# Performance work log

Measured on AMD Instinct MI355X. Metric: run time of the kernel, lower is better.

The kernel has to match this reference:

```python
import jax, jax.numpy as jnp
import numpy as np
from functools import partial

TAU = 2.0          # LIFNode default tau
V_TH = 1.0         # default v_threshold
ALPHA = 2.0        # SoftSign surrogate default alpha (unused in fwd; heaviside forward)

T, B, F = 256, 64, 1024


@jax.custom_vjp
def soft_sign_spike(x):
    # forward: heaviside; backward: SoftSign surrogate gradient
    return (x >= 0).astype(x.dtype)

def _sss_fwd(x):
    return (x >= 0).astype(x.dtype), x

def _sss_bwd(x, g):
    grad = g * (ALPHA / 2.0) / jnp.square(1.0 + jnp.abs(ALPHA * x))
    return (grad,)

soft_sign_spike.defvjp(_sss_fwd, _sss_bwd)


def setup_inputs() -> dict:
    key = jax.random.key(0)
    k1, k2 = jax.random.split(key)
    # binary input spikes, as an SNN would receive
    input_spikes = (jax.random.uniform(k1, (T, B, F)) < 0.5).astype(jnp.float32)
    # torch.nn.Linear weight [out_features, in_features], Kaiming-uniform-ish init
    bound = 1.0 / np.sqrt(F)
    W = jax.random.uniform(k2, (F, F), minval=-bound, maxval=bound, dtype=jnp.float32)
    return {"input_spikes": input_spikes, "W": W}


def reference(input_spikes, W):
    # batch the per-timestep Linear into one GEMM: y = x @ W.T
    cur = jnp.einsum("tbf,gf->tbg", input_spikes, W)  # [T, B, F]

    def step(v, x):
        # decay_input=True, v_reset=0: v = v + (x - v) / tau
        v = v + (x - v) / TAU
        s = soft_sign_spike(v - V_TH)
        # hard reset to v_reset=0 (detach_reset=False)
        v = (1.0 - s) * v
        return v, s

    v0 = jnp.zeros(cur.shape[1:], dtype=cur.dtype)
    _, out = jax.lax.scan(step, v0, cur)
    return out  # [T, B, F] output spikes
```

## Files before the change

kernel.cpp:

```cpp
#include <hip/hip_runtime.h>
#include <stdint.h>


#define T_STEPS 256
#define M_DIM 16384
#define N_DIM 1024
#define K_DIM 1024
#define PLANE 65536

typedef int v4i  __attribute__((ext_vector_type(4)));
typedef int v16i __attribute__((ext_vector_type(16)));
typedef unsigned int u32;
typedef unsigned long long u64;

#define AB_BYTES   (M_DIM * K_DIM)
#define AB_LIMB    AB_BYTES
#define WS_AB      (AB_BYTES + 4 * (1 << 20))
#define MT_BITS    (M_DIM * 128)
#define WS_MT      (MT_BITS + 4 * (1 << 20))

__device__ __forceinline__ void gload_lds16(const void* g, void* l) {
    __builtin_amdgcn_global_load_lds(
        (const __attribute__((address_space(1))) u32*)g,
        (__attribute__((address_space(3))) u32*)l, 16, 0, 0);
}

__global__ __launch_bounds__(256) void prep_bytes_f(const float* __restrict__ X,
                                                    uint4* __restrict__ af) {
    const int gid  = blockIdx.x * 256 + threadIdx.x;
    const int lane = gid & 63;
    const int fs   = gid >> 6;
    const int m    = (fs >> 5) * 32 + (lane & 31);
    const int k    = (fs & 31) * 32 + (lane >> 5) * 16;
    const float4* src = reinterpret_cast<const float4*>(X + (size_t)m * K_DIM + k);
    uint4 r;
    u32* pr = &r.x;
    #pragma unroll
    for (int q = 0; q < 4; ++q) {
        const float4 f = src[q];
        pr[q] = (f.x != 0.f ? 1u : 0u) | (f.y != 0.f ? 0x100u : 0u) |
                (f.z != 0.f ? 0x10000u : 0u) | (f.w != 0.f ? 0x1000000u : 0u);
    }
    af[gid] = r;
}

__global__ __launch_bounds__(256) void prep_limbs_f(const float* __restrict__ W,
                                                    char* __restrict__ bf) {
    const int gid  = blockIdx.x * 256 + threadIdx.x;
    const int lane = gid & 63;
    const int fs   = gid >> 6;
    const int n    = (fs >> 5) * 32 + (lane & 31);
    const int k    = (fs & 31) * 32 + (lane >> 5) * 16;
    const float* src = W + (size_t)n * K_DIM + k;
    u32 w0[4] = {}, w1[4] = {}, w2[4] = {}, w3[4] = {};
    #pragma unroll
    for (int e = 0; e < 16; ++e) {
        const double d = (double)src[e] * 34359738368.0;
        long long kq = llrint(d);
        const int8_t l0 = (int8_t)kq; kq = (kq - l0) >> 8;
        const int8_t l1 = (int8_t)kq; kq = (kq - l1) >> 8;
        const int8_t l2 = (int8_t)kq; kq = (kq - l2) >> 8;
        const int8_t l3 = (int8_t)kq;
        const int sh = (e & 3) * 8, wd = e >> 2;
        w0[wd] |= ((u32)(uint8_t)l0) << sh;
        w1[wd] |= ((u32)(uint8_t)l1) << sh;
        w2[wd] |= ((u32)(uint8_t)l2) << sh;
        w3[wd] |= ((u32)(uint8_t)l3) << sh;
    }
    char* base = bf + (size_t)fs * 4096 + lane * 16;
    *(uint4*)(base)        = make_uint4(w0[0], w0[1], w0[2], w0[3]);
    *(uint4*)(base + 1024) = make_uint4(w1[0], w1[1], w1[2], w1[3]);
    *(uint4*)(base + 2048) = make_uint4(w2[0], w2[1], w2[2], w2[3]);
    *(uint4*)(base + 3072) = make_uint4(w3[0], w3[1], w3[2], w3[3]);
}

__global__ __launch_bounds__(512, 4) void gemm_i8_w8(
    const char* __restrict__ af, const char* __restrict__ bf,
    float* __restrict__ out) {
    __shared__ __align__(16) char lds[2][16384];

    const int tid  = threadIdx.x;
    const int lane = tid & 63;
    const int w    = tid >> 6;
    const int l31  = lane & 31;
    const int lh   = lane >> 5;

    const int L   = blockIdx.x;
    const int xcd = L & 7;
    const int j   = L >> 3;
    const int bm  = xcd * 8 + (j & 7);
    const int bn  = j >> 3;

    v16i acc[4] = {};

    const char* gB = bf + (size_t)bn * 131072 + (size_t)(2 * w) * 1024 + lane * 16;

    const char* gA = af + (size_t)(bm * 8 + w) * 32768 + lane * 16;

    gload_lds16(gB,        (char*)lds[0] + (2 * w) * 1024 + lane * 16);
    gload_lds16(gB + 1024, (char*)lds[0] + (2 * w) * 1024 + 1024 + lane * 16);
    v4i aw = *(const v4i*)(gA);
    v4i an;
    __syncthreads();

    for (int c = 0; c < 8; ++c) {
        const char* rb = lds[c & 1];
        char* wb = (char*)lds[(c & 1) ^ 1];
        if (c < 7) {
            gload_lds16(gB + (size_t)(c + 1) * 16384,
                        wb + (2 * w) * 1024 + lane * 16);
            gload_lds16(gB + (size_t)(c + 1) * 16384 + 1024,
                        wb + (2 * w) * 1024 + 1024 + lane * 16);
        }
        #pragma unroll
        for (int ks = 0; ks < 4; ++ks) {
            const int kg = c * 4 + ks;
            if (kg + 1 < 32) an = *(const v4i*)(gA + (kg + 1) * 1024);
            #pragma unroll
            for (int lb = 0; lb < 4; ++lb) {
                const v4i b = *(const v4i*)(rb + (ks * 4 + lb) * 1024 + lane * 16);
                acc[lb] = __builtin_amdgcn_mfma_i32_32x32x32_i8(aw, b, acc[lb], 0, 0, 0);
            }
            aw = an;
        }
        __syncthreads();
    }

    const int n = bn * 32 + l31;
    #pragma unroll
    for (int r = 0; r < 16; ++r) {
        const double s = (double)acc[0][r] + 256.0 * (double)acc[1][r] +
                         65536.0 * (double)acc[2][r] +
                         16777216.0 * (double)acc[3][r];
        const float cur = (float)(s * 2.9103830456733704e-11);
        const int row = (r & 3) + 8 * (r >> 2) + 4 * lh;
        const int m = (bm * 8 + w) * 32 + row;
        out[(size_t)m * N_DIM + n] = cur;
    }
}

__device__ __forceinline__ v4i expand16(u32 sb) {
    v4i r;
    #pragma unroll
    for (int q = 0; q < 4; ++q) {
        const u32 x = (sb >> (4 * q)) & 0xFu;
        r[q] = (int)((x * 0x00204081u) & 0x01010101u);
    }
    return r;
}

__global__ __launch_bounds__(256) void prep_bits(const float* __restrict__ X,
                                                 u64* __restrict__ bits) {
    const int gid = blockIdx.x * 256 + threadIdx.x;
    const float x = X[gid];
    const u64 m = __ballot(x != 0.0f);
    if ((threadIdx.x & 63) == 0) bits[gid >> 6] = m;
}

__global__ __launch_bounds__(256) void prep_limbs(const float* __restrict__ W,
                                                  char* __restrict__ limbs) {
    const int gid = blockIdx.x * 256 + threadIdx.x;
    const double d = (double)W[gid] * 34359738368.0;
    long long k = llrint(d);
    const int8_t l0 = (int8_t)k; k = (k - l0) >> 8;
    const int8_t l1 = (int8_t)k; k = (k - l1) >> 8;
    const int8_t l2 = (int8_t)k; k = (k - l2) >> 8;
    const int8_t l3 = (int8_t)k;
    limbs[gid]                 = (char)l0;
    limbs[gid + (1 << 20)]     = (char)l1;
    limbs[gid + 2 * (1 << 20)] = (char)l2;
    limbs[gid + 3 * (1 << 20)] = (char)l3;
}

__global__ __launch_bounds__(256, 2) void gemm_i8_reg2(
    const u64* __restrict__ bits, const char* __restrict__ limbs,
    float* __restrict__ out) {
    __shared__ __align__(16) char lds[2][32768];
    const int tid  = threadIdx.x;
    const int lane = tid & 63;
    const int w    = tid >> 6;
    const int l31  = lane & 31;
    const int lh   = lane >> 5;
    const int bn   = blockIdx.x;
    const int bm   = blockIdx.y;
    v16i acc[2][4] = {};
    const char* gB[8];
    #pragma unroll
    for (int j = 0; j < 8; ++j) {
        const int id = w * 8 + j;
        const int lb = id & 3, ks32 = id >> 2;
        gB[j] = limbs + (size_t)lb * (1 << 20) +
                (size_t)(bn * 32 + l31) * 1024 + (size_t)(ks32 * 32 + lh * 16);
    }
    const int ldsbase = w * 8192 + lane * 16;
    const u64* aRow0 = bits + (size_t)(bm * 256 + w * 64 + l31) * 16;
    const u64* aRow1 = aRow0 + 32 * 16;
    u64 aw0[4], aw1[4], an0[4], an1[4];
    #pragma unroll
    for (int j = 0; j < 8; ++j) gload_lds16(gB[j], lds[0] + ldsbase + j * 1024);
    #pragma unroll
    for (int q = 0; q < 4; ++q) { aw0[q] = aRow0[q]; aw1[q] = aRow1[q]; }
    __syncthreads();
    char* rb = lds[0];
    char* wb = lds[1];
    for (int c = 0; c < 4; ++c) {
        if (c < 3) {
            #pragma unroll
            for (int j = 0; j < 8; ++j)
                gload_lds16(gB[j] + (c + 1) * 256, wb + ldsbase + j * 1024);
            #pragma unroll
            for (int q = 0; q < 4; ++q) {
                an0[q] = aRow0[(c + 1) * 4 + q];
                an1[q] = aRow1[(c + 1) * 4 + q];
            }
        }
        #pragma unroll
        for (int ks = 0; ks < 8; ++ks) {
            const int sh = (ks & 1) * 32 + lh * 16;
            const v4i a0 = expand16((u32)(aw0[ks >> 1] >> sh) & 0xffffu);
            const v4i a1 = expand16((u32)(aw1[ks >> 1] >> sh) & 0xffffu);
            #pragma unroll
            for (int lb = 0; lb < 4; ++lb) {
                const v4i b = *(const v4i*)(rb + (ks * 4 + lb) * 1024 + lane * 16);
                acc[0][lb] = __builtin_amdgcn_mfma_i32_32x32x32_i8(a0, b, acc[0][lb], 0, 0, 0);
                acc[1][lb] = __builtin_amdgcn_mfma_i32_32x32x32_i8(a1, b, acc[1][lb], 0, 0, 0);
            }
        }
        __syncthreads();
        char* t2 = rb; rb = wb; wb = t2;
        #pragma unroll
        for (int q = 0; q < 4; ++q) { aw0[q] = an0[q]; aw1[q] = an1[q]; }
    }
    const int n = bn * 32 + l31;
    #pragma unroll
    for (int i = 0; i < 2; ++i) {
        #pragma unroll
        for (int r = 0; r < 16; ++r) {
            const double s = (double)acc[i][0][r] + 256.0 * (double)acc[i][1][r] +
                             65536.0 * (double)acc[i][2][r] +
                             16777216.0 * (double)acc[i][3][r];
            const float cur = (float)(s * 2.9103830456733704e-11);
            const int row = (r & 3) + 8 * (r >> 2) + 4 * lh;
            const int m = bm * 256 + w * 64 + i * 32 + row;
            out[(size_t)m * N_DIM + n] = cur;
        }
    }
}

__global__ __launch_bounds__(256) void lif_scan4(float* __restrict__ buf) {
    const int gid = blockIdx.x * 256 + threadIdx.x;
    float c[16];
    #pragma unroll
    for (int q = 0; q < 16; ++q) c[q] = buf[(size_t)q * PLANE + gid];
    double v = 0.0;
    for (int t = 0; t < T_STEPS; t += 16) {
        #pragma unroll
        for (int q = 0; q < 16; ++q) {
            const double cd = (double)c[q];
            v = v + (cd - v) * 0.5;
            const bool s = (v >= 1.0);
            buf[(size_t)(t + q) * PLANE + gid] = s ? 1.0f : 0.0f;
            v = s ? 0.0 : v;
            const int tn = t + q + 16;
            if (tn < T_STEPS) c[q] = buf[(size_t)tn * PLANE + gid];
        }
    }
}

__global__ __launch_bounds__(256) void lif_gemm_fp64(
    const float* __restrict__ X, const float* __restrict__ W,
    float* __restrict__ out) {
    __shared__ float As[64][68];
    __shared__ float Bs[64][68];
    const int tid = threadIdx.x;
    const int bn = blockIdx.x, bm = blockIdx.y;
    const int tn4 = tid & 15, tm4 = tid >> 4;
    double acc[4][4] = {};
    const int lrow = tid >> 2, lc4 = tid & 3;
    const float* Abase = X + (size_t)(bm * 64 + lrow) * K_DIM;
    const float* Bbase = W + (size_t)(bn * 64 + lrow) * K_DIM;
    for (int k0 = 0; k0 < K_DIM; k0 += 64) {
        #pragma unroll
        for (int j = 0; j < 4; ++j) {
            const int c = lc4 + 4 * j;
            float4 a = *reinterpret_cast<const float4*>(Abase + k0 + 4 * c);
            float4 b = *reinterpret_cast<const float4*>(Bbase + k0 + 4 * c);
            As[4*c+0][lrow] = a.x; As[4*c+1][lrow] = a.y;
            As[4*c+2][lrow] = a.z; As[4*c+3][lrow] = a.w;
            Bs[4*c+0][lrow] = b.x; Bs[4*c+1][lrow] = b.y;
            Bs[4*c+2][lrow] = b.z; Bs[4*c+3][lrow] = b.w;
        }
        __syncthreads();
        #pragma unroll 8
        for (int k = 0; k < 64; ++k) {
            float4 a4 = *reinterpret_cast<const float4*>(&As[k][tm4 * 4]);
            float4 b4 = *reinterpret_cast<const float4*>(&Bs[k][tn4 * 4]);
            const double ad[4] = {(double)a4.x, (double)a4.y, (double)a4.z, (double)a4.w};
            const double bd[4] = {(double)b4.x, (double)b4.y, (double)b4.z, (double)b4.w};
            #pragma unroll
            for (int i = 0; i < 4; ++i)
                #pragma unroll
                for (int j = 0; j < 4; ++j)
                    acc[i][j] = fma(ad[i], bd[j], acc[i][j]);
        }
        __syncthreads();
    }
    #pragma unroll
    for (int i = 0; i < 4; ++i) {
        const int m = bm * 64 + tm4 * 4 + i;
        float4 o;
        o.x = (float)acc[i][0]; o.y = (float)acc[i][1];
        o.z = (float)acc[i][2]; o.w = (float)acc[i][3];
        *reinterpret_cast<float4*>(out + (size_t)m * N_DIM + bn * 64 + tn4 * 4) = o;
    }
}

extern "C" void kernel_launch(void* const* d_in, const int* in_sizes, int n_in,
                              void* d_out, int out_size, void* d_ws, size_t ws_size,
                              hipStream_t stream) {
    const float* X = (const float*)d_in[0];
    const float* W = (const float*)d_in[1];
    float* out = (float*)d_out;
    char* ws = (char*)d_ws;

    if (ws_size >= (size_t)WS_AB) {
        char* afrag = ws;
        char* bfrag = ws + AB_LIMB;
        prep_bytes_f<<<M_DIM * K_DIM / (256 * 16), 256, 0, stream>>>(X, (uint4*)afrag);
        prep_limbs_f<<<N_DIM * K_DIM / (256 * 16), 256, 0, stream>>>(W, bfrag);
        gemm_i8_w8<<<2048, 512, 0, stream>>>(afrag, bfrag, out);
    } else if (ws_size >= (size_t)WS_MT) {
        u64* bits = (u64*)ws;
        char* limbs = ws + MT_BITS;
        prep_bits<<<M_DIM * K_DIM / 256, 256, 0, stream>>>(X, bits);
        prep_limbs<<<N_DIM * K_DIM / 256, 256, 0, stream>>>(W, limbs);
        dim3 grid(N_DIM / 32, M_DIM / 256);
        gemm_i8_reg2<<<grid, 256, 0, stream>>>(bits, limbs, out);
    } else {
        dim3 grid(N_DIM / 64, M_DIM / 64);
        lif_gemm_fp64<<<grid, 256, 0, stream>>>(X, W, out);
        lif_scan4<<<PLANE / 256, 256, 0, stream>>>(out);
        return;
    }
    lif_scan4<<<PLANE / 256, 256, 0, stream>>>(out);
}
```

Baseline: 100.0 us.

## Triple-buffer B tiles in LDS with explicit vmcnt waits and deeper A prefetch

Replaces the double-buffered LDS pipeline in the int8 MFMA GEMM with a three-stage ring buffer. B tiles are now issued two chunks ahead, and the full __syncthreads is replaced by a partial s_waitcnt vmcnt plus s_barrier. A fragments are prefetched two k-steps ahead, and MFMA sections are wrapped in setprio. The aim is to hide global-to-LDS latency and barrier stalls, at the cost of 48KB LDS per block, which may reduce occupancy, and of relying on hand-counted vmcnt values for correctness.

```diff
diff --git a/kernel.cpp b/kernel.cpp
--- a/kernel.cpp
+++ b/kernel.cpp
@@ -74,10 +74,10 @@
     *(uint4*)(base + 3072) = make_uint4(w3[0], w3[1], w3[2], w3[3]);
 }
 
-__global__ __launch_bounds__(512, 4) void gemm_i8_w8(
+__global__ __launch_bounds__(512, 4) void gemm_i8_t4(
     const char* __restrict__ af, const char* __restrict__ bf,
     float* __restrict__ out) {
-    __shared__ __align__(16) char lds[2][16384];
+    __shared__ __align__(16) char lds[3][16384];
 
     const int tid  = threadIdx.x;
     const int lane = tid & 63;
@@ -94,36 +94,50 @@
     v16i acc[4] = {};
 
     const char* gB = bf + (size_t)bn * 131072 + (size_t)(2 * w) * 1024 + lane * 16;
+    const int   lB = (2 * w) * 1024 + lane * 16;
 
     const char* gA = af + (size_t)(bm * 8 + w) * 32768 + lane * 16;
 
-    gload_lds16(gB,        (char*)lds[0] + (2 * w) * 1024 + lane * 16);
-    gload_lds16(gB + 1024, (char*)lds[0] + (2 * w) * 1024 + 1024 + lane * 16);
-    v4i aw = *(const v4i*)(gA);
-    v4i an;
-    __syncthreads();
-
+    gload_lds16(gB,                 (char*)lds[0] + lB);
+    gload_lds16(gB + 1024,          (char*)lds[0] + lB + 1024);
+    gload_lds16(gB + 16384,         (char*)lds[1] + lB);
+    gload_lds16(gB + 16384 + 1024,  (char*)lds[1] + lB + 1024);
+    v4i a0 = *(const v4i*)(gA);
+    v4i a1 = *(const v4i*)(gA + 1024);
+    v4i a2 = a1;
+    __builtin_amdgcn_sched_barrier(0);
+    asm volatile("s_waitcnt vmcnt(4)" ::: "memory");
+    __builtin_amdgcn_s_barrier();
+    __builtin_amdgcn_sched_barrier(0);
+
+    #pragma unroll
     for (int c = 0; c < 8; ++c) {
-        const char* rb = lds[c & 1];
-        char* wb = (char*)lds[(c & 1) ^ 1];
-        if (c < 7) {
-            gload_lds16(gB + (size_t)(c + 1) * 16384,
-                        wb + (2 * w) * 1024 + lane * 16);
-            gload_lds16(gB + (size_t)(c + 1) * 16384 + 1024,
-                        wb + (2 * w) * 1024 + 1024 + lane * 16);
-        }
+        const char* rb = (const char*)lds[c % 3];
         #pragma unroll
         for (int ks = 0; ks < 4; ++ks) {
             const int kg = c * 4 + ks;
-            if (kg + 1 < 32) an = *(const v4i*)(gA + (kg + 1) * 1024);
+            if (kg + 2 < 32) a2 = *(const v4i*)(gA + (kg + 2) * 1024);
+            __builtin_amdgcn_s_setprio(1);
             #pragma unroll
             for (int lb = 0; lb < 4; ++lb) {
                 const v4i b = *(const v4i*)(rb + (ks * 4 + lb) * 1024 + lane * 16);
-                acc[lb] = __builtin_amdgcn_mfma_i32_32x32x32_i8(aw, b, acc[lb], 0, 0, 0);
+                acc[lb] = __builtin_amdgcn_mfma_i32_32x32x32_i8(a0, b, acc[lb], 0, 0, 0);
             }
-            aw = an;
-        }
-        __syncthreads();
+            __builtin_amdgcn_s_setprio(0);
+            a0 = a1; a1 = a2;
+        }
+        if (c < 7) {
+            __builtin_amdgcn_sched_barrier(0);
+            if (c + 2 < 8) {
+                char* wb2 = (char*)lds[(c + 2) % 3];
+                gload_lds16(gB + (size_t)(c + 2) * 16384,        wb2 + lB);
+                gload_lds16(gB + (size_t)(c + 2) * 16384 + 1024, wb2 + lB + 1024);
+            }
+            __builtin_amdgcn_sched_barrier(0);
+            asm volatile("s_waitcnt vmcnt(2)" ::: "memory");
+            __builtin_amdgcn_s_barrier();
+            __builtin_amdgcn_sched_barrier(0);
+        }
     }
 
     const int n = bn * 32 + l31;
@@ -328,7 +342,7 @@
         char* bfrag = ws + AB_LIMB;
         prep_bytes_f<<<M_DIM * K_DIM / (256 * 16), 256, 0, stream>>>(X, (uint4*)afrag);
         prep_limbs_f<<<N_DIM * K_DIM / (256 * 16), 256, 0, stream>>>(W, bfrag);
-        gemm_i8_w8<<<2048, 512, 0, stream>>>(afrag, bfrag, out);
+        gemm_i8_t4<<<2048, 512, 0, stream>>>(afrag, bfrag, out);
     } else if (ws_size >= (size_t)WS_MT) {
         u64* bits = (u64*)ws;
         char* limbs = ws + MT_BITS;
```

Measured after the change: 100.8 us. Within noise of the previous version (+0.7%).
